# Kernel optimization log

Hardware: AMD Instinct MI355X
Metric: run time of the kernel (lower is better)

## Reference

```python
import jax, jax.numpy as jnp
import numpy as np


def setup_inputs() -> dict:
    key = jax.random.key(0)
    B, F, H, W, C_out = 8, 64, 128, 128, 32
    V = H * W                     # grid vertices
    E = 3 * V                     # edges; flattened connectivity has 6V entries -> degree 6
    F2 = F // 2
    dim_channel = 6 * F2          # 192
    mid = dim_channel // 2        # 96
    out_ch = 2 * C_out            # 64
    k1, k2, k3, k4 = jax.random.split(key, 4)
    features = jax.random.normal(k1, (B, F, E), dtype=jnp.float32)
    # each vertex appears exactly 6 times in the flattened connectivity
    conn_flat = jax.random.permutation(k2, jnp.tile(jnp.arange(V, dtype=jnp.int32), 6))
    connectivity = conn_flat.reshape(E, 2)
    W1 = jax.random.normal(k3, (dim_channel, mid), dtype=jnp.float32) / np.sqrt(dim_channel)
    b1 = jnp.zeros((mid,), dtype=jnp.float32)
    W2 = jax.random.normal(k4, (mid, out_ch), dtype=jnp.float32) / np.sqrt(mid)
    b2 = jnp.zeros((out_ch,), dtype=jnp.float32)
    return {"features": features, "connectivity": connectivity,
            "output_dim": (H, W, C_out), "W1": W1, "b1": b1, "W2": W2, "b2": b2}


def _occurrence_rank(edges):
    # occ[i] = number of j < i with edges[j] == edges[i] (matches the serial
    # images_index bookkeeping in the torch loop). Stable argsort groups equal
    # vertices while preserving original order within a group.
    n = edges.shape[0]
    order = jnp.argsort(edges)            # stable by default in jax
    sorted_e = edges[order]
    first = jnp.searchsorted(sorted_e, sorted_e, side='left')
    rank_sorted = (jnp.arange(n) - first).astype(jnp.int32)
    return jnp.zeros(n, dtype=jnp.int32).at[order].set(rank_sorted)


def reference(features, connectivity, output_dim, W1, b1, W2, b2):
    B, F, E = features.shape
    H, Wd, C_out = int(output_dim[0]), int(output_dim[1]), int(output_dim[2])
    V = H * Wd
    F2 = F // 2
    edges = connectivity.reshape(-1)                      # [2E]
    # [B, F, E] -> [B, E, F] -> [B, 2E, F/2]: one half-feature per edge endpoint
    mesh = jnp.transpose(features, (0, 2, 1)).reshape(B, 2 * E, F2)
    occ = _occurrence_rank(edges)                         # slot per endpoint, 0..5
    # scatter half-features into [B, V, 6, F/2]; (vertex, slot) pairs are unique
    img = jnp.zeros((B, V, 6, F2), features.dtype).at[:, edges, occ, :].set(mesh)
    x = img.reshape(B, H, Wd, 6 * F2).transpose(0, 3, 1, 2)   # [B, 6*F/2, H, W]
    # 1x1 ConvTranspose2d == pointwise GEMM (torch weight layout [in, out, 1, 1])
    y = jax.nn.relu(jnp.einsum('bihw,io->bohw', x, W1) + b1[None, :, None, None])
    out = jax.nn.relu(jnp.einsum('bihw,io->bohw', y, W2) + b2[None, :, None, None])
    return out
```

## Files before the change

kernel.cpp:

```cpp
#include <hip/hip_runtime.h>
#include <hip/hip_bf16.h>
#include <stdint.h>

namespace {
constexpr int Bb   = 8;
constexpr int Ff   = 64;
constexpr int Ee   = 49152;
constexpr int Vv   = 16384;
constexpr int TWOE = 2 * Ee;
constexpr int MID  = 96;
constexpr int OUTC = 64;
}

typedef __attribute__((ext_vector_type(8))) short bf16x8;
typedef __attribute__((ext_vector_type(4))) float f32x4;
typedef __attribute__((ext_vector_type(4))) unsigned int u32x4;

__global__ void prep_misc(const float* __restrict__ W1, const float* __restrict__ W2,
                          __hip_bfloat16* __restrict__ w1f, __hip_bfloat16* __restrict__ w2f,
                          int* __restrict__ cnt) {
    int tid = blockIdx.x * 256 + threadIdx.x;
    if (tid < Vv) cnt[tid] = 0;
    if (tid < 18432) {
        int j = tid & 7, l = (tid >> 3) & 63, ft = tid >> 9;
        int kk = ft / 6, nt = ft - kk * 6;
        int k = kk * 32 + (l >> 4) * 8 + j;
        int n = nt * 16 + (l & 15);
        w1f[tid] = __float2bfloat16(W1[k * MID + n]);
    } else if (tid < 24576) {
        int t2 = tid - 18432;
        int j = t2 & 7, l = (t2 >> 3) & 63, ft = t2 >> 9;
        int kk = ft >> 2, nt = ft & 3;
        int k = kk * 32 + (l >> 4) * 8 + j;
        int n = nt * 16 + (l & 15);
        w2f[t2] = __float2bfloat16(W2[k * OUTC + n]);
    }
}

__global__ void bucket_fill(const int* __restrict__ conn, int* __restrict__ cnt,
                            int* __restrict__ buckets) {
    int i = blockIdx.x * 256 + threadIdx.x;
    if (i >= TWOE) return;
    int v = conn[i];
    int pos = atomicAdd(&cnt[v], 1);
    if (pos < 6) buckets[v * 6 + pos] = i;
}

__global__ void sort6_inv(const int* __restrict__ buckets, int* __restrict__ dest) {
    int v = blockIdx.x * 256 + threadIdx.x;
    if (v >= Vv) return;
    int a[6];
#pragma unroll
    for (int k = 0; k < 6; ++k) a[k] = buckets[v * 6 + k];
#define CSWAP(x, y) { int lo = min(a[x], a[y]); int hi = max(a[x], a[y]); a[x] = lo; a[y] = hi; }
    CSWAP(1, 2) CSWAP(4, 5) CSWAP(0, 2) CSWAP(3, 5) CSWAP(0, 1) CSWAP(3, 4)
    CSWAP(2, 5) CSWAP(0, 3) CSWAP(1, 4) CSWAP(2, 4) CSWAP(1, 3) CSWAP(2, 3)
#undef CSWAP
#pragma unroll
    for (int k = 0; k < 6; ++k) dest[a[k]] = v * 6 + k;
}

__global__ __launch_bounds__(256) void scatter_feats(const float* __restrict__ feat,
                                                     const int* __restrict__ dest,
                                                     ushort* __restrict__ xg) {
    __shared__ float tile[64][65];
    const int b  = blockIdx.y;
    const int e0 = blockIdx.x * 64;
    const int t  = threadIdx.x;
    const float* src = feat + (size_t)b * Ff * Ee;
    const int q  = t & 15;
    const int cb = t >> 4;
#pragma unroll
    for (int k = 0; k < 4; ++k) {
        int c = k * 16 + cb;
        float4 d = *reinterpret_cast<const float4*>(src + (size_t)c * Ee + e0 + q * 4);
        tile[c][q * 4 + 0] = d.x;
        tile[c][q * 4 + 1] = d.y;
        tile[c][q * 4 + 2] = d.z;
        tile[c][q * 4 + 3] = d.w;
    }
    __syncthreads();
    ushort* dst_base = xg + (size_t)b * ((size_t)Vv * 192);
#pragma unroll
    for (int it = 0; it < 2; ++it) {
        int item = it * 256 + t;
        int le = item >> 2, s2 = item & 3;
        int e = le >> 1, h = le & 1;
        int i = e0 * 2 + e * 2 + h;
        int d = dest[i];
        int c0 = h * 32 + s2 * 8;
        union { ushort u[8]; u32x4 qv; } pk;
#pragma unroll
        for (int k = 0; k < 8; ++k) {
            __hip_bfloat16 hv = __float2bfloat16(tile[c0 + k][e]);
            pk.u[k] = *reinterpret_cast<ushort*>(&hv);
        }
        *reinterpret_cast<u32x4*>(dst_base + (size_t)d * 32 + s2 * 8) = pk.qv;
    }
}

__global__ __launch_bounds__(256) void decode_mfma(
    const ushort* __restrict__ xg,
    const __hip_bfloat16* __restrict__ w1f, const float* __restrict__ b1,
    const __hip_bfloat16* __restrict__ w2f, const float* __restrict__ b2,
    float* __restrict__ out)
{
    __shared__ __align__(16) __hip_bfloat16 ys[64][104];
    const int t   = threadIdx.x;
    const int l   = t & 63;
    const int wid = t >> 6;
    const int b   = blockIdx.y;
    const int v0  = blockIdx.x * 64 + wid * 16;
    const int lr  = l & 15;
    const int lg  = l >> 4;

    const ushort* xv = xg + ((size_t)b * Vv + v0) * 192;

    f32x4 acc[6];
#pragma unroll
    for (int nt = 0; nt < 6; ++nt) {
        float bv = b1[nt * 16 + lr];
        acc[nt] = (f32x4){bv, bv, bv, bv};
    }
#pragma unroll
    for (int kk = 0; kk < 6; ++kk) {
        bf16x8 a = *reinterpret_cast<const bf16x8*>(xv + (size_t)lr * 192 + kk * 32 + lg * 8);
#pragma unroll
        for (int nt = 0; nt < 6; ++nt) {
            bf16x8 w = *reinterpret_cast<const bf16x8*>(w1f + ((size_t)((kk * 6 + nt) * 64 + l) * 8));
            acc[nt] = __builtin_amdgcn_mfma_f32_16x16x32_bf16(a, w, acc[nt], 0, 0, 0);
        }
    }
#pragma unroll
    for (int nt = 0; nt < 6; ++nt) {
#pragma unroll
        for (int r = 0; r < 4; ++r) {
            ys[wid * 16 + lg * 4 + r][nt * 16 + lr] = __float2bfloat16(fmaxf(acc[nt][r], 0.0f));
        }
    }
    __syncthreads();

    f32x4 acc2[4];
#pragma unroll
    for (int nt = 0; nt < 4; ++nt) {
        float bv = b2[nt * 16 + lr];
        acc2[nt] = (f32x4){bv, bv, bv, bv};
    }
#pragma unroll
    for (int kk = 0; kk < 3; ++kk) {
        bf16x8 a = *reinterpret_cast<const bf16x8*>(&ys[wid * 16 + lr][kk * 32 + lg * 8]);
#pragma unroll
        for (int nt = 0; nt < 4; ++nt) {
            bf16x8 w = *reinterpret_cast<const bf16x8*>(w2f + ((size_t)((kk * 4 + nt) * 64 + l) * 8));
            acc2[nt] = __builtin_amdgcn_mfma_f32_16x16x32_bf16(a, w, acc2[nt], 0, 0, 0);
        }
    }

    const int vbase = v0 + lg * 4;
#pragma unroll
    for (int nt = 0; nt < 4; ++nt) {
        f32x4 o4;
#pragma unroll
        for (int r = 0; r < 4; ++r) o4[r] = fmaxf(acc2[nt][r], 0.0f);
        *reinterpret_cast<f32x4*>(out + (((size_t)(b * OUTC + nt * 16 + lr)) << 14) + vbase) = o4;
    }
}

extern "C" void kernel_launch(void* const* d_in, const int* in_sizes, int n_in,
                              void* d_out, int out_size, void* d_ws, size_t ws_size,
                              hipStream_t stream) {
    const float* feat = (const float*)d_in[0];
    const int*   conn = (const int*)d_in[1];
    const float* W1   = (const float*)d_in[3];
    const float* b1   = (const float*)d_in[4];
    const float* W2   = (const float*)d_in[5];
    const float* b2   = (const float*)d_in[6];
    float* out = (float*)d_out;

    char* ws = (char*)d_ws;
    int* cnt     = (int*)ws;
    int* buckets = (int*)(ws + 65536);
    int* dest    = (int*)(ws + 65536 + 393216);
    __hip_bfloat16* w1f = (__hip_bfloat16*)(ws + 65536 + 2 * 393216);
    __hip_bfloat16* w2f = w1f + 18432;
    ushort* xg = (ushort*)(ws + 65536 + 2 * 393216 + 49152);

    prep_misc<<<96, 256, 0, stream>>>(W1, W2, w1f, w2f, cnt);
    bucket_fill<<<(TWOE + 255) / 256, 256, 0, stream>>>(conn, cnt, buckets);
    sort6_inv<<<(Vv + 255) / 256, 256, 0, stream>>>(buckets, dest);
    scatter_feats<<<dim3(Ee / 64, Bb), 256, 0, stream>>>(feat, dest, xg);
    decode_mfma<<<dim3(Vv / 64, Bb), 256, 0, stream>>>(xg, w1f, b1, w2f, b2, out);
}
```

Measured before the change: 65.78 us.

## Fuse prologue kernels into one cooperative kernel with grid syncs

```diff
diff --git a/kernel.cpp b/kernel.cpp
--- a/kernel.cpp
+++ b/kernel.cpp
@@ -1,6 +1,9 @@
 #include <hip/hip_runtime.h>
 #include <hip/hip_bf16.h>
+#include <hip/hip_cooperative_groups.h>
 #include <stdint.h>
+
+namespace cg = cooperative_groups;
 
 namespace {
 constexpr int Bb   = 8;
@@ -10,54 +13,57 @@
 constexpr int TWOE = 2 * Ee;
 constexpr int MID  = 96;
 constexpr int OUTC = 64;
+constexpr int PBLK = 384;
 }
 
 typedef __attribute__((ext_vector_type(8))) short bf16x8;
 typedef __attribute__((ext_vector_type(4))) float f32x4;
 typedef __attribute__((ext_vector_type(4))) unsigned int u32x4;
 
-__global__ void prep_misc(const float* __restrict__ W1, const float* __restrict__ W2,
-                          __hip_bfloat16* __restrict__ w1f, __hip_bfloat16* __restrict__ w2f,
-                          int* __restrict__ cnt) {
-    int tid = blockIdx.x * 256 + threadIdx.x;
-    if (tid < Vv) cnt[tid] = 0;
-    if (tid < 18432) {
-        int j = tid & 7, l = (tid >> 3) & 63, ft = tid >> 9;
+__global__ __launch_bounds__(256, 2) void prologue_coop(
+    const float* __restrict__ W1, const float* __restrict__ W2,
+    const int* __restrict__ conn,
+    __hip_bfloat16* __restrict__ w1f, __hip_bfloat16* __restrict__ w2f,
+    int* __restrict__ cnt, int* __restrict__ buckets, int* __restrict__ dest)
+{
+    cg::grid_group grid = cg::this_grid();
+    const int gtid = blockIdx.x * 256 + threadIdx.x;
+
+    if (gtid < Vv) cnt[gtid] = 0;
+    if (gtid < 18432) {
+        int j = gtid & 7, l = (gtid >> 3) & 63, ft = gtid >> 9;
         int kk = ft / 6, nt = ft - kk * 6;
         int k = kk * 32 + (l >> 4) * 8 + j;
         int n = nt * 16 + (l & 15);
-        w1f[tid] = __float2bfloat16(W1[k * MID + n]);
-    } else if (tid < 24576) {
-        int t2 = tid - 18432;
+        w1f[gtid] = __float2bfloat16(W1[k * MID + n]);
+    } else if (gtid < 24576) {
+        int t2 = gtid - 18432;
         int j = t2 & 7, l = (t2 >> 3) & 63, ft = t2 >> 9;
         int kk = ft >> 2, nt = ft & 3;
         int k = kk * 32 + (l >> 4) * 8 + j;
         int n = nt * 16 + (l & 15);
         w2f[t2] = __float2bfloat16(W2[k * OUTC + n]);
     }
-}
-
-__global__ void bucket_fill(const int* __restrict__ conn, int* __restrict__ cnt,
-                            int* __restrict__ buckets) {
-    int i = blockIdx.x * 256 + threadIdx.x;
-    if (i >= TWOE) return;
-    int v = conn[i];
-    int pos = atomicAdd(&cnt[v], 1);
-    if (pos < 6) buckets[v * 6 + pos] = i;
-}
-
-__global__ void sort6_inv(const int* __restrict__ buckets, int* __restrict__ dest) {
-    int v = blockIdx.x * 256 + threadIdx.x;
-    if (v >= Vv) return;
-    int a[6];
-#pragma unroll
-    for (int k = 0; k < 6; ++k) a[k] = buckets[v * 6 + k];
+    grid.sync();
+
+    {
+        int v = conn[gtid];
+        int pos = atomicAdd(&cnt[v], 1);
+        if (pos < 6) buckets[v * 6 + pos] = gtid;
+    }
+    grid.sync();
+
+    if (gtid < Vv) {
+        int a[6];
+#pragma unroll
+        for (int k = 0; k < 6; ++k) a[k] = buckets[gtid * 6 + k];
 #define CSWAP(x, y) { int lo = min(a[x], a[y]); int hi = max(a[x], a[y]); a[x] = lo; a[y] = hi; }
-    CSWAP(1, 2) CSWAP(4, 5) CSWAP(0, 2) CSWAP(3, 5) CSWAP(0, 1) CSWAP(3, 4)
-    CSWAP(2, 5) CSWAP(0, 3) CSWAP(1, 4) CSWAP(2, 4) CSWAP(1, 3) CSWAP(2, 3)
+        CSWAP(1, 2) CSWAP(4, 5) CSWAP(0, 2) CSWAP(3, 5) CSWAP(0, 1) CSWAP(3, 4)
+        CSWAP(2, 5) CSWAP(0, 3) CSWAP(1, 4) CSWAP(2, 4) CSWAP(1, 3) CSWAP(2, 3)
 #undef CSWAP
 #pragma unroll
-    for (int k = 0; k < 6; ++k) dest[a[k]] = v * 6 + k;
+        for (int k = 0; k < 6; ++k) dest[a[k]] = gtid * 6 + k;
+    }
 }
 
 __global__ __launch_bounds__(256) void scatter_feats(const float* __restrict__ feat,
@@ -185,9 +191,14 @@
     __hip_bfloat16* w2f = w1f + 18432;
     ushort* xg = (ushort*)(ws + 65536 + 2 * 393216 + 49152);
 
-    prep_misc<<<96, 256, 0, stream>>>(W1, W2, w1f, w2f, cnt);
-    bucket_fill<<<(TWOE + 255) / 256, 256, 0, stream>>>(conn, cnt, buckets);
-    sort6_inv<<<(Vv + 255) / 256, 256, 0, stream>>>(buckets, dest);
+    const float* W1c = W1; const float* W2c = W2; const int* connc = conn;
+    void* args[] = { (void*)&W1c, (void*)&W2c, (void*)&connc,
+                     (void*)&w1f, (void*)&w2f, (void*)&cnt,
+                     (void*)&buckets, (void*)&dest };
+    hipError_t err = hipLaunchCooperativeKernel((const void*)prologue_coop, dim3(PBLK),
+                                                dim3(256), args, 0, stream);
+    if (err != hipSuccess) {
+    }
     scatter_feats<<<dim3(Ee / 64, Bb), 256, 0, stream>>>(feat, dest, xg);
     decode_mfma<<<dim3(Vv / 64, Bb), 256, 0, stream>>>(xg, w1f, b1, w2f, b2, out);
 }
```

Measured after the change: 151.5 us. 130% more time.
